# Performance work log

Hardware: AMD Instinct MI355X
Metric: run time of the kernel (lower is better)

## Reference

```python
import jax, jax.numpy as jnp
import numpy as np

N_NODES = 10000
N_EDGES = 50000
DIM = 32
NHEAD = 4
HEAD_DIM = DIM // NHEAD
LN_EPS = 1e-5


def setup_inputs() -> dict:
    key = jax.random.key(0)
    ks = jax.random.split(key, 16)
    E, N, H, HD, D = N_EDGES, N_NODES, NHEAD, HEAD_DIM, DIM
    s = 1.0 / np.sqrt(D)
    return {
        "in_feat": jax.random.normal(ks[0], (N, D), jnp.float32),
        "src": jax.random.randint(ks[1], (E,), 0, N, jnp.int32),
        "dst": jax.random.randint(ks[2], (E,), 0, N, jnp.int32),
        "src_key_w": jax.random.normal(ks[3], (E, H, HD, D), jnp.float32) * s,
        "dst_key_w": jax.random.normal(ks[4], (E, H, HD, D), jnp.float32) * s,
        "src_key_b": jax.random.normal(ks[5], (E, H, HD), jnp.float32) * 0.02,
        "dst_key_b": jax.random.normal(ks[6], (E, H, HD), jnp.float32) * 0.02,
        "src_value_w": jax.random.normal(ks[7], (E, H, HD, D), jnp.float32) * s,
        "dst_value_w": jax.random.normal(ks[8], (E, H, HD, D), jnp.float32) * s,
        "src_value_b": jax.random.normal(ks[9], (E, H, HD), jnp.float32) * 0.02,
        "dst_value_b": jax.random.normal(ks[10], (E, H, HD), jnp.float32) * 0.02,
        "query": jax.random.normal(ks[11], (N, H, HD), jnp.float32) * s,
        "node_w": jax.random.normal(ks[12], (N, D, D), jnp.float32) * s,
        "node_b": jax.random.normal(ks[13], (N, D), jnp.float32) * 0.02,
        "ln_w": jnp.ones((D,), jnp.float32),
        "ln_b": jnp.zeros((D,), jnp.float32),
    }


def _layernorm(x, w, b):
    mu = jnp.mean(x, axis=-1, keepdims=True)
    var = jnp.mean(jnp.square(x - mu), axis=-1, keepdims=True)
    return (x - mu) * jax.lax.rsqrt(var + LN_EPS) * w + b


def reference(in_feat, src, dst, src_key_w, dst_key_w, src_key_b, dst_key_b,
              src_value_w, dst_value_w, src_value_b, dst_value_b,
              query, node_w, node_b, ln_w, ln_b):
    N = in_feat.shape[0]
    E = src.shape[0]
    u = in_feat[src]          # (E, D) source node feature per edge
    v = in_feat[dst]          # (E, D) destination node feature per edge

    # edgewise dynamic-weight linear: per-edge hypernetwork matmuls
    K = (jnp.einsum('ehdi,ei->ehd', src_key_w, u) + src_key_b
         + jnp.einsum('ehdi,ei->ehd', dst_key_w, v) + dst_key_b)   # (E, H, HD)
    V = (jnp.einsum('ehdi,ei->ehd', src_value_w, u) + src_value_b
         + jnp.einsum('ehdi,ei->ehd', dst_value_w, v) + dst_value_b)  # (E, H, HD)

    # e_dot_v(KEY, QUERY): per-edge per-head dot with dst-node query
    logits = jnp.einsum('ehd,ehd->eh', K, query[dst])  # (E, H)

    # edge_softmax over incoming edges of each dst node, per head
    m = jax.ops.segment_max(logits, dst, num_segments=N)   # (N, H)
    ex = jnp.exp(logits - m[dst])
    denom = jax.ops.segment_sum(ex, dst, num_segments=N)   # (N, H)
    attn = ex / denom[dst]                                  # (E, H)

    # weighted scatter-sum aggregation into dst nodes
    agg = jax.ops.segment_sum(V * attn[..., None], dst, num_segments=N)  # (N, H, HD)
    agg = agg.reshape(N, -1)  # (N, D)

    # nodewise dynamic linear + relu
    out = jnp.einsum('noi,ni->no', node_w, agg) + node_b
    out = jax.nn.relu(out)

    # residual + layernorm
    out = _layernorm(in_feat + out, ln_w, ln_b)

    key_feat = K.reshape(E, -1)
    value_feat = V.reshape(E, -1)
    return out, key_feat, value_feat, attn
```

## Files before the change

### kernel.cpp

```cpp
#include <hip/hip_runtime.h>
#include <math.h>

constexpr int N = 10000;
constexpr int E = 50000;
constexpr int D = 32;
constexpr int H = 4;

__global__ __launch_bounds__(256) void edge_kernel(
    const float* __restrict__ in_feat,
    const int*   __restrict__ src, const int* __restrict__ dst,
    const float* __restrict__ skw, const float* __restrict__ dkw,
    const float* __restrict__ skb, const float* __restrict__ dkb,
    const float* __restrict__ svw, const float* __restrict__ dvw,
    const float* __restrict__ svb, const float* __restrict__ dvb,
    const float* __restrict__ query,
    float* __restrict__ key_feat, float* __restrict__ value_feat,
    float* __restrict__ ex_out,
    float* __restrict__ denom)
{
    const int e   = blockIdx.x;
    const int tid = threadIdx.x;
    const int hd  = tid >> 3;
    const int seg = tid & 7;
    const int s = src[e];
    const int d = dst[e];

    const float4 u4 = *reinterpret_cast<const float4*>(in_feat + s * D + seg * 4);
    const float4 v4 = *reinterpret_cast<const float4*>(in_feat + d * D + seg * 4);

    const size_t woff = (size_t)e * 1024 + (size_t)tid * 4;

    float4 wa = *reinterpret_cast<const float4*>(skw + woff);
    float4 wb = *reinterpret_cast<const float4*>(dkw + woff);
    float pk = wa.x * u4.x + wa.y * u4.y + wa.z * u4.z + wa.w * u4.w
             + wb.x * v4.x + wb.y * v4.y + wb.z * v4.z + wb.w * v4.w;
    wa = *reinterpret_cast<const float4*>(svw + woff);
    wb = *reinterpret_cast<const float4*>(dvw + woff);
    float pv = wa.x * u4.x + wa.y * u4.y + wa.z * u4.z + wa.w * u4.w
             + wb.x * v4.x + wb.y * v4.y + wb.z * v4.z + wb.w * v4.w;

    #pragma unroll
    for (int off = 1; off < 8; off <<= 1) {
        pk += __shfl_xor(pk, off);
        pv += __shfl_xor(pv, off);
    }

    const int bi = e * D + hd;
    const float Kv = pk + skb[bi] + dkb[bi];
    const float Vv = pv + svb[bi] + dvb[bi];
    if (seg == 0) {
        key_feat[bi]   = Kv;
        value_feat[bi] = Vv;
    }

    float c = Kv * query[d * D + hd];
    #pragma unroll
    for (int off = 8; off < 64; off <<= 1) c += __shfl_xor(c, off);

    if ((tid & 63) == 0) {
        const int h = tid >> 6;
        const float exv = expf(c);
        ex_out[e * H + h] = exv;
        atomicAdd(denom + d * H + h, exv);
    }
}

__global__ __launch_bounds__(256) void attn_kernel(
    const int*   __restrict__ dst,
    const float* __restrict__ value_feat,
    const float* __restrict__ denom,
    float* __restrict__ attn,
    float* __restrict__ agg)
{
    const int idx = blockIdx.x * 256 + threadIdx.x;
    if (idx >= E * H) return;
    const int e = idx >> 2;
    const int h = idx & 3;
    const int d = dst[e];
    const float a = attn[idx] / denom[d * H + h];
    attn[idx] = a;
    const float* vp = value_feat + e * D + h * 8;
    float*       ap = agg + d * D + h * 8;
    #pragma unroll
    for (int j = 0; j < 8; ++j) atomicAdd(ap + j, vp[j] * a);
}

__global__ __launch_bounds__(256) void node_kernel(
    const float* __restrict__ in_feat,
    const float* __restrict__ node_w,
    const float* __restrict__ node_b,
    const float* __restrict__ ln_w, const float* __restrict__ ln_b,
    const float* __restrict__ agg,
    float* __restrict__ out)
{
    const int wave = threadIdx.x >> 6;
    const int lane = threadIdx.x & 63;
    const int n = blockIdx.x * 4 + wave;
    if (n >= N) return;
    const int o    = lane >> 1;
    const int half = lane & 1;

    const float* w = node_w + (size_t)n * 1024 + o * 32 + half * 16;
    const float* g = agg + n * D + half * 16;
    float p = 0.f;
    #pragma unroll
    for (int j = 0; j < 16; j += 4) {
        const float4 wv = *reinterpret_cast<const float4*>(w + j);
        const float4 gv = *reinterpret_cast<const float4*>(g + j);
        p += wv.x * gv.x + wv.y * gv.y + wv.z * gv.z + wv.w * gv.w;
    }
    p += __shfl_xor(p, 1);

    const float r = in_feat[n * D + o] + fmaxf(p + node_b[n * D + o], 0.0f);

    float sum = r, sq = r * r;
    #pragma unroll
    for (int off = 2; off < 64; off <<= 1) {
        sum += __shfl_xor(sum, off);
        sq  += __shfl_xor(sq, off);
    }
    const float mean = sum * (1.0f / 32.0f);
    const float var  = sq * (1.0f / 32.0f) - mean * mean;
    const float y = (r - mean) * rsqrtf(var + 1e-5f) * ln_w[o] + ln_b[o];
    if (half == 0) out[n * D + o] = y;
}

extern "C" void kernel_launch(void* const* d_in, const int* in_sizes, int n_in,
                              void* d_out, int out_size, void* d_ws, size_t ws_size,
                              hipStream_t stream)
{
    const float* in_feat = (const float*)d_in[0];
    const int*   src     = (const int*)d_in[1];
    const int*   dst     = (const int*)d_in[2];
    const float* skw     = (const float*)d_in[3];
    const float* dkw     = (const float*)d_in[4];
    const float* skb     = (const float*)d_in[5];
    const float* dkb     = (const float*)d_in[6];
    const float* svw     = (const float*)d_in[7];
    const float* dvw     = (const float*)d_in[8];
    const float* svb     = (const float*)d_in[9];
    const float* dvb     = (const float*)d_in[10];
    const float* query   = (const float*)d_in[11];
    const float* node_w  = (const float*)d_in[12];
    const float* node_b  = (const float*)d_in[13];
    const float* ln_w    = (const float*)d_in[14];
    const float* ln_b    = (const float*)d_in[15];

    float* out        = (float*)d_out;
    float* key_feat   = out + (size_t)N * D;
    float* value_feat = key_feat + (size_t)E * D;
    float* attn       = value_feat + (size_t)E * D;

    float* denom = (float*)d_ws;
    float* agg   = denom + N * H;
    hipMemsetAsync(d_ws, 0, (size_t)(N * H + N * D) * sizeof(float), stream);

    edge_kernel<<<E, 256, 0, stream>>>(in_feat, src, dst,
                                       skw, dkw, skb, dkb,
                                       svw, dvw, svb, dvb,
                                       query, key_feat, value_feat,
                                       attn , denom);

    attn_kernel<<<(E * H + 255) / 256, 256, 0, stream>>>(dst, value_feat,
                                                         denom, attn, agg);

    node_kernel<<<(N + 3) / 4, 256, 0, stream>>>(in_feat, node_w, node_b,
                                                 ln_w, ln_b, agg, out);
}
```

Baseline: 745.3 us.

## Build CSR by destination and fuse softmax/aggregation into node kernel

Adds histogram, scan and scatter kernels that build a destination-sorted edge list. The per-node softmax normalisation and weighted aggregation move into the node kernel, which removes the float atomics on denom and agg and drops the separate attention kernel. The edge kernel also issues all four weight loads up front as nontemporal loads. The cost is three extra small launches, including a single-block scan, plus serial per-node loops whose work depends on node degree.

```diff
diff --git a/kernel.cpp b/kernel.cpp
--- a/kernel.cpp
+++ b/kernel.cpp
@@ -5,6 +5,62 @@
 constexpr int E = 50000;
 constexpr int D = 32;
 constexpr int H = 4;
+
+typedef float v4f __attribute__((ext_vector_type(4)));
+
+__global__ __launch_bounds__(256) void hist_kernel(const int* __restrict__ dst,
+                                                   int* __restrict__ counts)
+{
+    const int e = blockIdx.x * 256 + threadIdx.x;
+    if (e < E) atomicAdd(counts + dst[e], 1);
+}
+
+__global__ __launch_bounds__(1024) void scan_kernel(const int* __restrict__ counts,
+                                                    int* __restrict__ offsets,
+                                                    int* __restrict__ cursor)
+{
+    __shared__ int part[1024];
+    const int t = threadIdx.x;
+    constexpr int PER = (N + 1023) / 1024;
+    const int base = t * PER;
+    int loc[PER];
+    int s = 0;
+    #pragma unroll
+    for (int i = 0; i < PER; ++i) {
+        const int c = (base + i < N) ? counts[base + i] : 0;
+        loc[i] = s;
+        s += c;
+    }
+    part[t] = s;
+    __syncthreads();
+    for (int off = 1; off < 1024; off <<= 1) {
+        const int v = (t >= off) ? part[t - off] : 0;
+        __syncthreads();
+        part[t] += v;
+        __syncthreads();
+    }
+    const int pre = (t == 0) ? 0 : part[t - 1];
+    #pragma unroll
+    for (int i = 0; i < PER; ++i) {
+        if (base + i < N) {
+            const int o = pre + loc[i];
+            offsets[base + i] = o;
+            cursor[base + i]  = o;
+        }
+    }
+    if (t == 0) offsets[N] = E;
+}
+
+__global__ __launch_bounds__(256) void scatter_kernel(const int* __restrict__ dst,
+                                                      int* __restrict__ cursor,
+                                                      int* __restrict__ edge_list)
+{
+    const int e = blockIdx.x * 256 + threadIdx.x;
+    if (e < E) {
+        const int p = atomicAdd(cursor + dst[e], 1);
+        edge_list[p] = e;
+    }
+}
 
 __global__ __launch_bounds__(256) void edge_kernel(
     const float* __restrict__ in_feat,
@@ -15,8 +71,7 @@
     const float* __restrict__ svb, const float* __restrict__ dvb,
     const float* __restrict__ query,
     float* __restrict__ key_feat, float* __restrict__ value_feat,
-    float* __restrict__ ex_out,
-    float* __restrict__ denom)
+    float* __restrict__ ex_out)
 {
     const int e   = blockIdx.x;
     const int tid = threadIdx.x;
@@ -29,15 +84,15 @@
     const float4 v4 = *reinterpret_cast<const float4*>(in_feat + d * D + seg * 4);
 
     const size_t woff = (size_t)e * 1024 + (size_t)tid * 4;
-
-    float4 wa = *reinterpret_cast<const float4*>(skw + woff);
-    float4 wb = *reinterpret_cast<const float4*>(dkw + woff);
+    const v4f wa = __builtin_nontemporal_load(reinterpret_cast<const v4f*>(skw + woff));
+    const v4f wb = __builtin_nontemporal_load(reinterpret_cast<const v4f*>(dkw + woff));
+    const v4f wc = __builtin_nontemporal_load(reinterpret_cast<const v4f*>(svw + woff));
+    const v4f wd = __builtin_nontemporal_load(reinterpret_cast<const v4f*>(dvw + woff));
+
     float pk = wa.x * u4.x + wa.y * u4.y + wa.z * u4.z + wa.w * u4.w
              + wb.x * v4.x + wb.y * v4.y + wb.z * v4.z + wb.w * v4.w;
-    wa = *reinterpret_cast<const float4*>(svw + woff);
-    wb = *reinterpret_cast<const float4*>(dvw + woff);
-    float pv = wa.x * u4.x + wa.y * u4.y + wa.z * u4.z + wa.w * u4.w
-             + wb.x * v4.x + wb.y * v4.y + wb.z * v4.z + wb.w * v4.w;
+    float pv = wc.x * u4.x + wc.y * u4.y + wc.z * u4.z + wc.w * u4.w
+             + wd.x * v4.x + wd.y * v4.y + wd.z * v4.z + wd.w * v4.w;
 
     #pragma unroll
     for (int off = 1; off < 8; off <<= 1) {
@@ -46,68 +101,79 @@
     }
 
     const int bi = e * D + hd;
-    const float Kv = pk + skb[bi] + dkb[bi];
-    const float Vv = pv + svb[bi] + dvb[bi];
+    float c = 0.0f;
     if (seg == 0) {
+        const float Kv = pk + skb[bi] + dkb[bi];
+        const float Vv = pv + svb[bi] + dvb[bi];
         key_feat[bi]   = Kv;
         value_feat[bi] = Vv;
-    }
-
-    float c = Kv * query[d * D + hd];
+        c = Kv * query[d * D + hd];
+    }
     #pragma unroll
     for (int off = 8; off < 64; off <<= 1) c += __shfl_xor(c, off);
 
     if ((tid & 63) == 0) {
         const int h = tid >> 6;
-        const float exv = expf(c);
-        ex_out[e * H + h] = exv;
-        atomicAdd(denom + d * H + h, exv);
-    }
-}
-
-__global__ __launch_bounds__(256) void attn_kernel(
-    const int*   __restrict__ dst,
-    const float* __restrict__ value_feat,
-    const float* __restrict__ denom,
+        ex_out[e * H + h] = expf(c);
+    }
+}
+
+__global__ __launch_bounds__(256) void node_kernel(
+    const int*   __restrict__ offsets, const int* __restrict__ edge_list,
+    const float* __restrict__ in_feat, const float* __restrict__ value_feat,
+    const float* __restrict__ node_w,  const float* __restrict__ node_b,
+    const float* __restrict__ ln_w,    const float* __restrict__ ln_b,
     float* __restrict__ attn,
-    float* __restrict__ agg)
-{
-    const int idx = blockIdx.x * 256 + threadIdx.x;
-    if (idx >= E * H) return;
-    const int e = idx >> 2;
-    const int h = idx & 3;
-    const int d = dst[e];
-    const float a = attn[idx] / denom[d * H + h];
-    attn[idx] = a;
-    const float* vp = value_feat + e * D + h * 8;
-    float*       ap = agg + d * D + h * 8;
-    #pragma unroll
-    for (int j = 0; j < 8; ++j) atomicAdd(ap + j, vp[j] * a);
-}
-
-__global__ __launch_bounds__(256) void node_kernel(
-    const float* __restrict__ in_feat,
-    const float* __restrict__ node_w,
-    const float* __restrict__ node_b,
-    const float* __restrict__ ln_w, const float* __restrict__ ln_b,
-    const float* __restrict__ agg,
     float* __restrict__ out)
 {
+    __shared__ float agg_sh[4][33];
     const int wave = threadIdx.x >> 6;
     const int lane = threadIdx.x & 63;
     const int n = blockIdx.x * 4 + wave;
-    if (n >= N) return;
-    const int o    = lane >> 1;
-    const int half = lane & 1;
-
+
+    const int beg = offsets[n];
+    const int deg = offsets[n + 1] - beg;
+
+    const int slot = lane >> 2;
+    const int hh   = lane & 3;
+    const int hd   = lane & 31;
+    const int h    = hd >> 3;
+
+    float ds = 0.0f;
+    for (int k = slot; k < deg; k += 16)
+        ds += attn[edge_list[beg + k] * H + hh];
+    #pragma unroll
+    for (int off = 4; off < 64; off <<= 1) ds += __shfl_xor(ds, off);
+    const float rden = (ds != 0.0f) ? 1.0f / ds : 0.0f;
+
+    float aggv = 0.0f;
+    for (int c = 0; c < deg; c += 16) {
+        const int rem = (deg - c < 16) ? (deg - c) : 16;
+        int   ee = 0;
+        float a  = 0.0f;
+        if (slot < rem) {
+            ee = edge_list[beg + c + slot];
+            const int idx = ee * H + hh;
+            a = attn[idx] * rden;
+            attn[idx] = a;
+        }
+        for (int kk = 0; kk < rem; ++kk) {
+            const float ak = __shfl(a, kk * 4 + h);
+            const int  ek = __shfl(ee, kk * 4);
+            aggv += value_feat[ek * D + hd] * ak;
+        }
+    }
+    agg_sh[wave][hd] = aggv;
+    __syncthreads();
+
+    const int o = lane >> 1, half = lane & 1;
     const float* w = node_w + (size_t)n * 1024 + o * 32 + half * 16;
-    const float* g = agg + n * D + half * 16;
-    float p = 0.f;
+    const float* g = &agg_sh[wave][half * 16];
+    float p = 0.0f;
     #pragma unroll
     for (int j = 0; j < 16; j += 4) {
         const float4 wv = *reinterpret_cast<const float4*>(w + j);
-        const float4 gv = *reinterpret_cast<const float4*>(g + j);
-        p += wv.x * gv.x + wv.y * gv.y + wv.z * gv.z + wv.w * gv.w;
+        p += wv.x * g[j] + wv.y * g[j + 1] + wv.z * g[j + 2] + wv.w * g[j + 3];
     }
     p += __shfl_xor(p, 1);
 
@@ -151,19 +217,23 @@
     float* value_feat = key_feat + (size_t)E * D;
     float* attn       = value_feat + (size_t)E * D;
 
-    float* denom = (float*)d_ws;
-    float* agg   = denom + N * H;
-    hipMemsetAsync(d_ws, 0, (size_t)(N * H + N * D) * sizeof(float), stream);
+    int* counts    = (int*)d_ws;
+    int* offsets   = counts + N;
+    int* cursor    = offsets + (N + 1);
+    int* edge_list = cursor + N;
+
+    hipMemsetAsync(counts, 0, (size_t)N * sizeof(int), stream);
+    hist_kernel<<<(E + 255) / 256, 256, 0, stream>>>(dst, counts);
+    scan_kernel<<<1, 1024, 0, stream>>>(counts, offsets, cursor);
+    scatter_kernel<<<(E + 255) / 256, 256, 0, stream>>>(dst, cursor, edge_list);
 
     edge_kernel<<<E, 256, 0, stream>>>(in_feat, src, dst,
                                        skw, dkw, skb, dkb,
                                        svw, dvw, svb, dvb,
-                                       query, key_feat, value_feat,
-                                       attn , denom);
-
-    attn_kernel<<<(E * H + 255) / 256, 256, 0, stream>>>(dst, value_feat,
-                                                         denom, attn, agg);
-
-    node_kernel<<<(N + 3) / 4, 256, 0, stream>>>(in_feat, node_w, node_b,
-                                                 ln_w, ln_b, agg, out);
-}
+                                       query, key_feat, value_feat, attn);
+
+    node_kernel<<<N / 4, 256, 0, stream>>>(offsets, edge_list,
+                                           in_feat, value_feat,
+                                           node_w, node_b, ln_w, ln_b,
+                                           attn, out);
+}
```

Measured after the change: 707.0 us. 5.1% less time.
